# Kernel tuning notes

Hardware: AMD Instinct MI355X
Metric: run time of the kernel (lower is better)

## Reference

```python
import jax, jax.numpy as jnp
import numpy as np

D_MODEL = 512
OUT_MODEL = 512
NUM_HEADS = 8
D_K = OUT_MODEL // NUM_HEADS


def setup_inputs() -> dict:
    key = jax.random.key(0)
    ks = jax.random.split(key, 11)
    B, S = 4, 2048
    inp = {
        "Q": jax.random.normal(ks[0], (B, S, D_MODEL), dtype=jnp.float32),
        "K": jax.random.normal(ks[1], (B, S, D_MODEL), dtype=jnp.float32),
        "V": jax.random.normal(ks[2], (B, S, D_MODEL), dtype=jnp.float32),
    }
    sc = 1.0 / np.sqrt(D_MODEL)
    inp["Wq"] = jax.random.normal(ks[3], (D_MODEL, OUT_MODEL), dtype=jnp.float32) * sc
    inp["bq"] = jnp.zeros((OUT_MODEL,), dtype=jnp.float32)
    inp["Wk"] = jax.random.normal(ks[4], (D_MODEL, OUT_MODEL), dtype=jnp.float32) * sc
    inp["bk"] = jnp.zeros((OUT_MODEL,), dtype=jnp.float32)
    inp["Wv"] = jax.random.normal(ks[5], (D_MODEL, OUT_MODEL), dtype=jnp.float32) * sc
    inp["bv"] = jnp.zeros((OUT_MODEL,), dtype=jnp.float32)
    inp["Wo"] = jax.random.normal(ks[6], (OUT_MODEL, OUT_MODEL), dtype=jnp.float32) * sc
    inp["bo"] = jnp.zeros((OUT_MODEL,), dtype=jnp.float32)
    return inp


def _split_heads(x):
    B, S, _ = x.shape
    return x.reshape(B, S, NUM_HEADS, D_K).transpose(0, 2, 1, 3)  # [B,H,S,Dk]


def reference(Q, K, V, Wq, bq, Wk, bk, Wv, bv, Wo, bo):
    q = _split_heads(Q @ Wq + bq)
    k = _split_heads(K @ Wk + bk)
    v = _split_heads(V @ Wv + bv)
    scores = jnp.einsum("bhsd,bhtd->bhst", q, k) / jnp.sqrt(jnp.float32(D_K))
    probs = jax.nn.softmax(scores, axis=-1)
    attn = jnp.einsum("bhst,bhtd->bhsd", probs, v)  # [B,H,S,Dk]
    B, H, S, Dk = attn.shape
    merged = attn.transpose(0, 2, 1, 3).reshape(B, S, OUT_MODEL)
    return merged @ Wo + bo
```

## Files before the change

kernel.cpp:

```cpp
#include <hip/hip_runtime.h>
#include <hip/hip_bf16.h>
#include <cstdint>


using short8 = __attribute__((ext_vector_type(8))) short;
using f32x4  = __attribute__((ext_vector_type(4))) float;
using f32x16 = __attribute__((ext_vector_type(16))) float;

#define DEVINL __device__ __forceinline__

constexpr int BB  = 4;
constexpr int SS  = 2048;
constexpr int DM  = 512;
constexpr int NH  = 8;
constexpr int DKH = 64;
constexpr float C2 = 0.18033688011112042f;

DEVINL unsigned short f2bf(float f) {
    __hip_bfloat16 h = __float2bfloat16(f);
    return *reinterpret_cast<unsigned short*>(&h);
}

DEVINL f32x4 mfma16(short8 a, short8 b, f32x4 c) {
    return __builtin_amdgcn_mfma_f32_16x16x32_bf16(a, b, c, 0, 0, 0);
}
DEVINL f32x16 mfma32(short8 a, short8 b, f32x16 c) {
    return __builtin_amdgcn_mfma_f32_32x32x16_bf16(a, b, c, 0, 0, 0);
}

DEVINL void gl16(const void* g, void* l) {
    __builtin_amdgcn_global_load_lds(
        (const __attribute__((address_space(1))) unsigned int*)g,
        (__attribute__((address_space(3))) unsigned int*)l, 16, 0, 0);
}
DEVINL void vmcnt0() { asm volatile("s_waitcnt vmcnt(0)" ::: "memory"); }

DEVINL unsigned cvtpk(float a, float b) {
    unsigned r;
    asm("v_cvt_pk_bf16_f32 %0, %1, %2" : "=v"(r) : "v"(a), "v"(b));
    return r;
}

__global__ __launch_bounds__(256)
void prep_w(const float* __restrict__ Wq, const float* __restrict__ Wk,
            const float* __restrict__ Wv, const float* __restrict__ Wo,
            unsigned short* __restrict__ wt)
{
    const int z = blockIdx.z;
    const float* W = (z == 0) ? Wq : (z == 1) ? Wk : (z == 2) ? Wv : Wo;
    unsigned short* Wtz = wt + (size_t)z * DM * DM;

    __shared__ unsigned short T[64][72];
    const int t = threadIdx.x;
    const int k0 = blockIdx.x * 64, n0 = blockIdx.y * 64;
    const int r = t >> 2, cs = t & 3;

    #pragma unroll
    for (int q = 0; q < 4; ++q) {
        float4 v = *reinterpret_cast<const float4*>(
            &W[(size_t)(k0 + r) * DM + n0 + cs * 16 + q * 4]);
        union { unsigned short u[4]; unsigned long long ll; } pk;
        pk.u[0] = f2bf(v.x); pk.u[1] = f2bf(v.y);
        pk.u[2] = f2bf(v.z); pk.u[3] = f2bf(v.w);
        *reinterpret_cast<unsigned long long*>(&T[r][cs * 16 + q * 4]) = pk.ll;
    }
    __syncthreads();
    union { unsigned short u[8]; short8 v; } p0, p1;
    #pragma unroll
    for (int e = 0; e < 8; ++e) p0.u[e] = T[cs * 16 + e][r];
    #pragma unroll
    for (int e = 0; e < 8; ++e) p1.u[e] = T[cs * 16 + 8 + e][r];
    *reinterpret_cast<short8*>(&Wtz[(size_t)(n0 + r) * DM + k0 + cs * 16]) = p0.v;
    *reinterpret_cast<short8*>(&Wtz[(size_t)(n0 + r) * DM + k0 + cs * 16 + 8]) = p1.v;
}

__global__ __launch_bounds__(256, 4)
void qkv_proj_kernel(const float* __restrict__ Qin, const float* __restrict__ Kin,
                     const float* __restrict__ Vin,
                     const unsigned short* __restrict__ wt,
                     const float* __restrict__ bq, const float* __restrict__ bk,
                     const float* __restrict__ bv,
                     unsigned short* __restrict__ qb, unsigned short* __restrict__ kb,
                     unsigned short* __restrict__ vt)
{
    const int z = blockIdx.z;
    const float* A           = (z == 0) ? Qin : (z == 1) ? Kin : Vin;
    const unsigned short* Wt = wt + (size_t)z * DM * DM;
    const float* bias        = (z == 0) ? bq : (z == 1) ? bk : bv;

    __shared__ unsigned short As[2][128][32];
    __shared__ unsigned short Bs[2][128][32];

    const int tid = threadIdx.x, lane = tid & 63, w = tid >> 6;
    const int wm = w >> 1, wn = w & 1;
    const int row16 = lane & 15, kg = lane >> 4;
    const int m0tok = blockIdx.x * 128, n0ch = blockIdx.y * 128;

    const int ar = tid >> 1, ah = tid & 1;

    float4 apf[4];
    auto load_A = [&](int kt) {
        const float* Ap = &A[(size_t)(m0tok + ar) * DM + kt * 32 + ah * 16];
        #pragma unroll
        for (int q = 0; q < 4; ++q)
            apf[q] = *reinterpret_cast<const float4*>(Ap + q * 4);
    };
    auto write_A = [&](int buf) {
        #pragma unroll
        for (int s = 0; s < 2; ++s) {
            union { unsigned short u[8]; short8 v; } pk;
            float4 a = apf[2 * s], b = apf[2 * s + 1];
            pk.u[0] = f2bf(a.x); pk.u[1] = f2bf(a.y);
            pk.u[2] = f2bf(a.z); pk.u[3] = f2bf(a.w);
            pk.u[4] = f2bf(b.x); pk.u[5] = f2bf(b.y);
            pk.u[6] = f2bf(b.z); pk.u[7] = f2bf(b.w);
            int phys = (ah * 2 + s) ^ (ar & 3);
            *reinterpret_cast<short8*>(&As[buf][ar][phys * 8]) = pk.v;
        }
    };
    auto issue_B = [&](int kt, int buf) {
        #pragma unroll
        for (int i = 0; i < 2; ++i) {
            int chunk = tid + i * 256;
            int n = chunk >> 2, c = chunk & 3;
            const unsigned short* src =
                &Wt[(size_t)(n0ch + n) * DM + kt * 32 + ((c ^ (n & 3)) * 8)];
            gl16(src, (char*)&Bs[buf][0][0] + (size_t)(w * 64 + i * 256) * 16);
        }
    };

    f32x4 acc[4][4] = {};
    const int aoff = ((z == 2) ? wn : wm) * 64;
    const int boff = ((z == 2) ? wm : wn) * 64;

    load_A(0); issue_B(0, 0);
    vmcnt0();
    write_A(0);
    __syncthreads();

    for (int t = 0; t < 16; ++t) {
        const int cur = t & 1, nxt = cur ^ 1;
        if (t + 1 < 16) { issue_B(t + 1, nxt); load_A(t + 1); }

        short8 af[4], bfr[4];
        #pragma unroll
        for (int i = 0; i < 4; ++i) {
            int ra = aoff + i * 16 + row16;
            int rb = boff + i * 16 + row16;
            af[i]  = *reinterpret_cast<const short8*>(
                &As[cur][ra][((kg ^ (ra & 3)) * 8)]);
            bfr[i] = *reinterpret_cast<const short8*>(
                &Bs[cur][rb][((kg ^ (rb & 3)) * 8)]);
        }
        __builtin_amdgcn_s_setprio(1);
        #pragma unroll
        for (int mf = 0; mf < 4; ++mf)
            #pragma unroll
            for (int nf = 0; nf < 4; ++nf)
                acc[mf][nf] = (z == 2)
                    ? mfma16(bfr[mf], af[nf], acc[mf][nf])
                    : mfma16(af[mf], bfr[nf], acc[mf][nf]);
        __builtin_amdgcn_s_setprio(0);

        vmcnt0();
        if (t + 1 < 16) write_A(nxt);
        __syncthreads();
    }

    if (z < 2) {
        unsigned short* C = (z == 0) ? qb : kb;
        const float osc = (z == 0) ? C2 : 1.0f;
        #pragma unroll
        for (int nf = 0; nf < 4; ++nf) {
            int ch = n0ch + wn * 64 + nf * 16 + row16;
            float bval = bias[ch];
            int h = ch >> 6, dk = ch & 63;
            #pragma unroll
            for (int mf = 0; mf < 4; ++mf)
                #pragma unroll
                for (int j = 0; j < 4; ++j) {
                    int tok = m0tok + wm * 64 + mf * 16 + kg * 4 + j;
                    int b = tok >> 11, s = tok & 2047;
                    C[(((size_t)b * NH + h) * SS + s) * DKH + dk] =
                        f2bf((acc[mf][nf][j] + bval) * osc);
                }
        }
    } else {
        #pragma unroll
        for (int mf = 0; mf < 4; ++mf)
            #pragma unroll
            for (int j = 0; j < 4; ++j) {
                int ch = n0ch + wm * 64 + mf * 16 + kg * 4 + j;
                float bval = bias[ch];
                int h = ch >> 6, dk = ch & 63;
                #pragma unroll
                for (int nf = 0; nf < 4; ++nf) {
                    int tok = m0tok + wn * 64 + nf * 16 + row16;
                    int b = tok >> 11, s = tok & 2047;
                    vt[(((size_t)b * NH + h) * DKH + dk) * SS + s] =
                        f2bf(acc[mf][nf][j] + bval);
                }
            }
    }
}

__global__ __launch_bounds__(256, 3)
void attn_kernel(const unsigned short* __restrict__ qb,
                 const unsigned short* __restrict__ kb,
                 const unsigned short* __restrict__ vt,
                 unsigned short* __restrict__ am)
{
    __shared__ unsigned short Qs[128][64];
    __shared__ unsigned short Ks[2][64][64];
    __shared__ unsigned short Vs[2][64][64];

    const int tid = threadIdx.x, lane = tid & 63, w = tid >> 6;
    const int l31 = lane & 31, hi = lane >> 5;
    const int bh = blockIdx.y, b = bh >> 3, h = bh & 7;
    const int q0 = blockIdx.x * 128;
    const size_t base = (size_t)bh * SS * DKH;

    auto stage_KV = [&](int t0, int buf) {
        #pragma unroll
        for (int i = 0; i < 2; ++i) {
            int cc = tid + i * 256;
            int r = cc >> 3, c = cc & 7;
            gl16(&kb[base + (size_t)(t0 + r) * DKH + ((c ^ (r & 7)) * 8)],
                 (char*)&Ks[buf][0][0] + (size_t)(w * 64 + i * 256) * 16);
            gl16(&vt[base + (size_t)r * SS + t0 + ((c ^ (r & 7)) * 8)],
                 (char*)&Vs[buf][0][0] + (size_t)(w * 64 + i * 256) * 16);
        }
    };

    #pragma unroll
    for (int i = 0; i < 4; ++i) {
        int cc = tid + i * 256;
        int r = cc >> 3, c = cc & 7;
        gl16(&qb[base + (size_t)(q0 + r) * DKH + ((c ^ (r & 7)) * 8)],
             (char*)&Qs[0][0] + (size_t)(w * 64 + i * 256) * 16);
    }
    stage_KV(0, 0);
    vmcnt0();
    __syncthreads();

    short8 qf[4];
    const int qrow = w * 32 + l31;
    #pragma unroll
    for (int ks = 0; ks < 4; ++ks) {
        int c = ks * 2 + hi;
        qf[ks] = *reinterpret_cast<const short8*>(
            &Qs[qrow][((c ^ (qrow & 7)) * 8)]);
    }

    f32x16 o[2] = {};
    float lsum = 0.f;

    for (int t0 = 0; t0 < SS; t0 += 64) {
        const int cur = (t0 >> 6) & 1;
        if (t0 + 64 < SS) stage_KV(t0 + 64, cur ^ 1);

        f32x16 sfr[2] = {};
        __builtin_amdgcn_s_setprio(1);
        #pragma unroll
        for (int ks = 0; ks < 4; ++ks)
            #pragma unroll
            for (int mkv = 0; mkv < 2; ++mkv) {
                int row = mkv * 32 + l31;
                int c = ks * 2 + hi;
                short8 kf = *reinterpret_cast<const short8*>(
                    &Ks[cur][row][((c ^ (row & 7)) * 8)]);
                sfr[mkv] = mfma32(kf, qf[ks], sfr[mkv]);
            }
        __builtin_amdgcn_s_setprio(0);

        unsigned pk[2][4][2];
        #pragma unroll
        for (int mkv = 0; mkv < 2; ++mkv)
            #pragma unroll
            for (int bq = 0; bq < 4; ++bq) {
                float p0 = __builtin_amdgcn_exp2f(sfr[mkv][bq * 4 + 0]);
                float p1 = __builtin_amdgcn_exp2f(sfr[mkv][bq * 4 + 1]);
                float p2 = __builtin_amdgcn_exp2f(sfr[mkv][bq * 4 + 2]);
                float p3 = __builtin_amdgcn_exp2f(sfr[mkv][bq * 4 + 3]);
                lsum += (p0 + p1) + (p2 + p3);
                pk[mkv][bq][0] = cvtpk(p0, p1);
                pk[mkv][bq][1] = cvtpk(p2, p3);
            }

        __builtin_amdgcn_s_setprio(1);
        #pragma unroll
        for (int ks2 = 0; ks2 < 4; ++ks2) {
            const int mkv = ks2 >> 1, b0 = (ks2 & 1) * 2, b1 = b0 + 1;
            unsigned x0 = pk[mkv][b0][0], y0 = pk[mkv][b1][0];
            unsigned x1 = pk[mkv][b0][1], y1 = pk[mkv][b1][1];
            asm volatile("v_permlane32_swap_b32 %0, %1" : "+v"(x0), "+v"(y0));
            asm volatile("v_permlane32_swap_b32 %0, %1" : "+v"(x1), "+v"(y1));
            union { unsigned u[4]; short8 s; } pa;
            pa.u[0] = x0; pa.u[1] = x1; pa.u[2] = y0; pa.u[3] = y1;
            #pragma unroll
            for (int ndk = 0; ndk < 2; ++ndk) {
                int row = ndk * 32 + l31;
                int c = ks2 * 2 + hi;
                short8 vf = *reinterpret_cast<const short8*>(
                    &Vs[cur][row][((c ^ (row & 7)) * 8)]);
                o[ndk] = mfma32(pa.s, vf, o[ndk]);
            }
        }
        __builtin_amdgcn_s_setprio(0);

        vmcnt0();
        __syncthreads();
    }

    float lfull = lsum + __shfl_xor(lsum, 32, 64);
    float linv = 1.0f / lfull;
    #pragma unroll
    for (int r = 0; r < 16; ++r) {
        int qloc = (r & 3) + 8 * (r >> 2) + 4 * hi;
        float li = __shfl(linv, qloc, 64);
        int sg = q0 + w * 32 + qloc;
        #pragma unroll
        for (int ndk = 0; ndk < 2; ++ndk) {
            int dk = ndk * 32 + l31;
            am[((size_t)b * SS + sg) * DM + h * DKH + dk] =
                f2bf(o[ndk][r] * li);
        }
    }
}

__global__ __launch_bounds__(256, 4)
void out_proj_kernel(const unsigned short* __restrict__ am,
                     const unsigned short* __restrict__ Wt,
                     const float* __restrict__ bo,
                     float* __restrict__ out)
{
    __shared__ unsigned short As[2][128][32];
    __shared__ unsigned short Bs[2][128][32];

    const int tid = threadIdx.x, lane = tid & 63, w = tid >> 6;
    const int wm = w >> 1, wn = w & 1;
    const int row16 = lane & 15, kg = lane >> 4;
    const int m0 = blockIdx.x * 128;
    const int n0 = blockIdx.y * 128;

    auto issue_AB = [&](int kt, int buf) {
        #pragma unroll
        for (int i = 0; i < 2; ++i) {
            int chunk = tid + i * 256;
            int r = chunk >> 2, c = chunk & 3;
            gl16(&am[(size_t)(m0 + r) * DM + kt * 32 + ((c ^ (r & 3)) * 8)],
                 (char*)&As[buf][0][0] + (size_t)(w * 64 + i * 256) * 16);
            gl16(&Wt[(size_t)(n0 + r) * DM + kt * 32 + ((c ^ (r & 3)) * 8)],
                 (char*)&Bs[buf][0][0] + (size_t)(w * 64 + i * 256) * 16);
        }
    };

    f32x4 acc[4][4] = {};

    issue_AB(0, 0);
    vmcnt0();
    __syncthreads();

    for (int t = 0; t < 16; ++t) {
        const int cur = t & 1, nxt = cur ^ 1;
        if (t + 1 < 16) issue_AB(t + 1, nxt);

        short8 af[4], bfr[4];
        #pragma unroll
        for (int i = 0; i < 4; ++i) {
            int ra = wm * 64 + i * 16 + row16;
            int rb = wn * 64 + i * 16 + row16;
            af[i]  = *reinterpret_cast<const short8*>(
                &As[cur][ra][((kg ^ (ra & 3)) * 8)]);
            bfr[i] = *reinterpret_cast<const short8*>(
                &Bs[cur][rb][((kg ^ (rb & 3)) * 8)]);
        }
        __builtin_amdgcn_s_setprio(1);
        #pragma unroll
        for (int mf = 0; mf < 4; ++mf)
            #pragma unroll
            for (int nf = 0; nf < 4; ++nf)
                acc[mf][nf] = mfma16(af[mf], bfr[nf], acc[mf][nf]);
        __builtin_amdgcn_s_setprio(0);

        vmcnt0();
        __syncthreads();
    }

    #pragma unroll
    for (int nf = 0; nf < 4; ++nf) {
        int n = n0 + wn * 64 + nf * 16 + row16;
        float bval = bo[n];
        #pragma unroll
        for (int mf = 0; mf < 4; ++mf)
            #pragma unroll
            for (int j = 0; j < 4; ++j) {
                int mrow = m0 + wm * 64 + mf * 16 + kg * 4 + j;
                out[(size_t)mrow * DM + n] = acc[mf][nf][j] + bval;
            }
    }
}

extern "C" void kernel_launch(void* const* d_in, const int* in_sizes, int n_in,
                              void* d_out, int out_size, void* d_ws, size_t ws_size,
                              hipStream_t stream) {
    const float* Q  = (const float*)d_in[0];
    const float* K  = (const float*)d_in[1];
    const float* V  = (const float*)d_in[2];
    const float* Wq = (const float*)d_in[3];
    const float* bq = (const float*)d_in[4];
    const float* Wk = (const float*)d_in[5];
    const float* bk = (const float*)d_in[6];
    const float* Wv = (const float*)d_in[7];
    const float* bv = (const float*)d_in[8];
    const float* Wo = (const float*)d_in[9];
    const float* bo = (const float*)d_in[10];
    float* out = (float*)d_out;

    const size_t per = (size_t)BB * NH * SS * DKH;
    unsigned short* qb = (unsigned short*)d_ws;
    unsigned short* kb = qb + per;
    unsigned short* vt = kb + per;
    unsigned short* am = vt + per;
    unsigned short* wt = am + per;

    prep_w<<<dim3(8, 8, 4), 256, 0, stream>>>(Wq, Wk, Wv, Wo, wt);
    qkv_proj_kernel<<<dim3(64, 4, 3), 256, 0, stream>>>(
        Q, K, V, wt, bq, bk, bv, qb, kb, vt);
    attn_kernel<<<dim3(SS / 128, BB * NH), 256, 0, stream>>>(qb, kb, vt, am);
    out_proj_kernel<<<dim3(64, 4), 256, 0, stream>>>(
        am, wt + 3 * (size_t)DM * DM, bo, out);
}
```

Measured before the change: 96.79 us.

## Triple-buffer attention K/V loads and halve out-proj M tile

The attention kernel moves from double to triple buffering of K/V tiles with a prefetch distance of two. It uses partial vmcnt waits and a raw s_barrier instead of draining all loads each iteration, and the launch bound drops to 2 blocks per CU to fit the extra LDS. Separately, the output projection uses 64-row M tiles with twice as many blocks to improve occupancy and CU fill. The risks are lower attention occupancy and more redundant weight loads in the projection.

```diff
diff --git a/kernel.cpp b/kernel.cpp
--- a/kernel.cpp
+++ b/kernel.cpp
@@ -34,6 +34,8 @@
         (__attribute__((address_space(3))) unsigned int*)l, 16, 0, 0);
 }
 DEVINL void vmcnt0() { asm volatile("s_waitcnt vmcnt(0)" ::: "memory"); }
+#define WAIT_VM(N) asm volatile("s_waitcnt vmcnt(" #N ")" ::: "memory")
+DEVINL void barrier() { __builtin_amdgcn_s_barrier(); }
 
 DEVINL unsigned cvtpk(float a, float b) {
     unsigned r;
@@ -204,15 +206,15 @@
     }
 }
 
-__global__ __launch_bounds__(256, 3)
+__global__ __launch_bounds__(256, 2)
 void attn_kernel(const unsigned short* __restrict__ qb,
                  const unsigned short* __restrict__ kb,
                  const unsigned short* __restrict__ vt,
                  unsigned short* __restrict__ am)
 {
     __shared__ unsigned short Qs[128][64];
-    __shared__ unsigned short Ks[2][64][64];
-    __shared__ unsigned short Vs[2][64][64];
+    __shared__ unsigned short Ks[3][64 * 64];
+    __shared__ unsigned short Vs[3][64 * 64];
 
     const int tid = threadIdx.x, lane = tid & 63, w = tid >> 6;
     const int l31 = lane & 31, hi = lane >> 5;
@@ -226,9 +228,9 @@
             int cc = tid + i * 256;
             int r = cc >> 3, c = cc & 7;
             gl16(&kb[base + (size_t)(t0 + r) * DKH + ((c ^ (r & 7)) * 8)],
-                 (char*)&Ks[buf][0][0] + (size_t)(w * 64 + i * 256) * 16);
+                 (char*)Ks + (size_t)buf * 8192 + (size_t)(w * 64 + i * 256) * 16);
             gl16(&vt[base + (size_t)r * SS + t0 + ((c ^ (r & 7)) * 8)],
-                 (char*)&Vs[buf][0][0] + (size_t)(w * 64 + i * 256) * 16);
+                 (char*)Vs + (size_t)buf * 8192 + (size_t)(w * 64 + i * 256) * 16);
         }
     };
 
@@ -240,8 +242,9 @@
              (char*)&Qs[0][0] + (size_t)(w * 64 + i * 256) * 16);
     }
     stage_KV(0, 0);
-    vmcnt0();
-    __syncthreads();
+    stage_KV(64, 1);
+    WAIT_VM(4);
+    barrier();
 
     short8 qf[4];
     const int qrow = w * 32 + l31;
@@ -255,9 +258,9 @@
     f32x16 o[2] = {};
     float lsum = 0.f;
 
-    for (int t0 = 0; t0 < SS; t0 += 64) {
-        const int cur = (t0 >> 6) & 1;
-        if (t0 + 64 < SS) stage_KV(t0 + 64, cur ^ 1);
+    for (int tt = 0; tt < 32; ++tt) {
+        const int cur = tt % 3;
+        if (tt + 2 < 32) stage_KV((tt + 2) * 64, (tt + 2) % 3);
 
         f32x16 sfr[2] = {};
         __builtin_amdgcn_s_setprio(1);
@@ -268,7 +271,7 @@
                 int row = mkv * 32 + l31;
                 int c = ks * 2 + hi;
                 short8 kf = *reinterpret_cast<const short8*>(
-                    &Ks[cur][row][((c ^ (row & 7)) * 8)]);
+                    &Ks[cur][row * 64 + ((c ^ (row & 7)) * 8)]);
                 sfr[mkv] = mfma32(kf, qf[ks], sfr[mkv]);
             }
         __builtin_amdgcn_s_setprio(0);
@@ -302,14 +305,15 @@
                 int row = ndk * 32 + l31;
                 int c = ks2 * 2 + hi;
                 short8 vf = *reinterpret_cast<const short8*>(
-                    &Vs[cur][row][((c ^ (row & 7)) * 8)]);
+                    &Vs[cur][row * 64 + ((c ^ (row & 7)) * 8)]);
                 o[ndk] = mfma32(pa.s, vf, o[ndk]);
             }
         }
         __builtin_amdgcn_s_setprio(0);
 
-        vmcnt0();
-        __syncthreads();
+        if (tt + 2 < 32)      { WAIT_VM(4); }
+        else if (tt + 1 < 32) { WAIT_VM(0); }
+        if (tt + 1 < 32) barrier();
     }
 
     float lfull = lsum + __shfl_xor(lsum, 32, 64);
@@ -334,50 +338,56 @@
                      const float* __restrict__ bo,
                      float* __restrict__ out)
 {
-    __shared__ unsigned short As[2][128][32];
-    __shared__ unsigned short Bs[2][128][32];
+    __shared__ unsigned short As[2][64 * 32];
+    __shared__ unsigned short Bs[2][128 * 32];
 
     const int tid = threadIdx.x, lane = tid & 63, w = tid >> 6;
-    const int wm = w >> 1, wn = w & 1;
+    const int wm = w & 1, wn = w >> 1;
     const int row16 = lane & 15, kg = lane >> 4;
-    const int m0 = blockIdx.x * 128;
+    const int m0 = blockIdx.x * 64;
     const int n0 = blockIdx.y * 128;
 
-    auto issue_AB = [&](int kt, int buf) {
+    auto stage = [&](int kt, int buf) {
+        {
+            int r = tid >> 2, c = tid & 3;
+            gl16(&am[(size_t)(m0 + r) * DM + kt * 32 + ((c ^ (r & 3)) * 8)],
+                 (char*)As + (size_t)buf * 4096 + (size_t)(w * 64) * 16);
+        }
         #pragma unroll
         for (int i = 0; i < 2; ++i) {
-            int chunk = tid + i * 256;
-            int r = chunk >> 2, c = chunk & 3;
-            gl16(&am[(size_t)(m0 + r) * DM + kt * 32 + ((c ^ (r & 3)) * 8)],
-                 (char*)&As[buf][0][0] + (size_t)(w * 64 + i * 256) * 16);
-            gl16(&Wt[(size_t)(n0 + r) * DM + kt * 32 + ((c ^ (r & 3)) * 8)],
-                 (char*)&Bs[buf][0][0] + (size_t)(w * 64 + i * 256) * 16);
+            int cc = tid + i * 256;
+            int n = cc >> 2, c = cc & 3;
+            gl16(&Wt[(size_t)(n0 + n) * DM + kt * 32 + ((c ^ (n & 3)) * 8)],
+                 (char*)Bs + (size_t)buf * 8192 + (size_t)(w * 64 + i * 256) * 16);
         }
     };
 
-    f32x4 acc[4][4] = {};
-
-    issue_AB(0, 0);
+    f32x4 acc[2][4] = {};
+
+    stage(0, 0);
     vmcnt0();
     __syncthreads();
 
     for (int t = 0; t < 16; ++t) {
         const int cur = t & 1, nxt = cur ^ 1;
-        if (t + 1 < 16) issue_AB(t + 1, nxt);
-
-        short8 af[4], bfr[4];
+        if (t + 1 < 16) stage(t + 1, nxt);
+
+        short8 af[2], bfr[4];
+        #pragma unroll
+        for (int i = 0; i < 2; ++i) {
+            int ra = wm * 32 + i * 16 + row16;
+            af[i] = *reinterpret_cast<const short8*>(
+                &As[cur][ra * 32 + ((kg ^ (ra & 3)) * 8)]);
+        }
         #pragma unroll
         for (int i = 0; i < 4; ++i) {
-            int ra = wm * 64 + i * 16 + row16;
             int rb = wn * 64 + i * 16 + row16;
-            af[i]  = *reinterpret_cast<const short8*>(
-                &As[cur][ra][((kg ^ (ra & 3)) * 8)]);
             bfr[i] = *reinterpret_cast<const short8*>(
-                &Bs[cur][rb][((kg ^ (rb & 3)) * 8)]);
+                &Bs[cur][rb * 32 + ((kg ^ (rb & 3)) * 8)]);
         }
         __builtin_amdgcn_s_setprio(1);
         #pragma unroll
-        for (int mf = 0; mf < 4; ++mf)
+        for (int mf = 0; mf < 2; ++mf)
             #pragma unroll
             for (int nf = 0; nf < 4; ++nf)
                 acc[mf][nf] = mfma16(af[mf], bfr[nf], acc[mf][nf]);
@@ -392,10 +402,10 @@
         int n = n0 + wn * 64 + nf * 16 + row16;
         float bval = bo[n];
         #pragma unroll
-        for (int mf = 0; mf < 4; ++mf)
+        for (int mf = 0; mf < 2; ++mf)
             #pragma unroll
             for (int j = 0; j < 4; ++j) {
-                int mrow = m0 + wm * 64 + mf * 16 + kg * 4 + j;
+                int mrow = m0 + wm * 32 + mf * 16 + kg * 4 + j;
                 out[(size_t)mrow * DM + n] = acc[mf][nf][j] + bval;
             }
     }
@@ -428,6 +438,6 @@
     qkv_proj_kernel<<<dim3(64, 4, 3), 256, 0, stream>>>(
         Q, K, V, wt, bq, bk, bv, qb, kb, vt);
     attn_kernel<<<dim3(SS / 128, BB * NH), 256, 0, stream>>>(qb, kb, vt, am);
-    out_proj_kernel<<<dim3(64, 4), 256, 0, stream>>>(
+    out_proj_kernel<<<dim3(128, 4), 256, 0, stream>>>(
         am, wt + 3 * (size_t)DM * DM, bo, out);
 }
```

Result: faster. 94.11 us (-2.8%).
